# Performance work log

Hardware: AMD Instinct MI355X
Metric: run time of the kernel (lower is better)

## Reference

```python
import jax, jax.numpy as jnp
import numpy as np

T, N, L, H, COND, VOCAB = 64, 1024, 16, 256, 64, 100
HC = H + 1  # task_encoder hidden = hidden_size + 1
STATE = 1 + 1 + H + L + L  # a, v, h, a_probs, p


def gru_step(x, h, w_ih, w_hh, b_ih, b_hh):
    # PyTorch GRU/GRUCell gate math
    gi = x @ w_ih.T + b_ih
    gh = h @ w_hh.T + b_hh
    ir, iz, ig = jnp.split(gi, 3, axis=-1)
    hr, hz, hg = jnp.split(gh, 3, axis=-1)
    r = jax.nn.sigmoid(ir + hr)
    z = jax.nn.sigmoid(iz + hz)
    n = jnp.tanh(ig + r * hg)
    return (1.0 - z) * n + z * h


def setup_inputs():
    ks = jax.random.split(jax.random.key(0), 20)
    g = lambda i, sh: jax.random.normal(ks[i], sh, jnp.float32) * 0.05
    return {
        "condition": jax.random.normal(ks[0], (T, N, COND), jnp.float32),
        "lines": jax.random.randint(ks[1], (N, L), 0, VOCAB),
        "actions": jax.random.randint(ks[2], (T, N), 0, L),
        "rnn_hxs": jnp.zeros((N, STATE), jnp.float32),
        "emb": g(3, (VOCAB, H)),
        "w_ih_enc": g(4, (3 * HC, H)), "w_hh_enc": g(5, (3 * HC, HC)),
        "b_ih_enc": g(6, (3 * HC,)), "b_hh_enc": g(7, (3 * HC,)),
        "W1": g(8, (H, COND + H)), "b1": g(9, (H,)),
        "W2": g(10, (H, H)), "b2": g(11, (H,)),
        "w_ih_cell": g(12, (3 * H, H)), "w_hh_cell": g(13, (3 * H, H)),
        "b_ih_cell": g(14, (3 * H,)), "b_hh_cell": g(15, (3 * H,)),
        "Wa": g(16, (H, H)), "ba": g(17, (H,)),
        "Wc": g(18, (1, H)), "bc": g(19, (1,)),
    }


def _forward(condition, rnn_hxs, emb, w_ih_enc, w_hh_enc, b_ih_enc, b_hh_enc,
             W1, b1, W2, b2, w_ih_cell, w_hh_cell, b_ih_cell, b_hh_cell,
             Wa, ba, Wc, bc, lines, actions):
    n, l = lines.shape
    M = emb[lines]                     # [N, L, H]
    seq = jnp.transpose(M, (1, 0, 2))  # [L, N, H]
    idx = jnp.arange(l)

    # backward encoder: single scan over reversed sequence (outputs are causal,
    # so they equal torch's task_encoder(backward_input[:i]) for every i)
    def bstep(h, x):
        h2 = gru_step(x, h, w_ih_enc, w_hh_enc, b_ih_enc, b_hh_enc)
        return h2, h2
    _, B = jax.lax.scan(bstep, jnp.zeros((n, HC), M.dtype), seq[::-1])  # [L, N, HC]

    # forward encoder from every start i, batched over i with a start mask
    def fstep(carry, xj):
        x, j = xj
        h2 = gru_step(x, carry, w_ih_enc, w_hh_enc, b_ih_enc, b_hh_enc)  # [L(i), N, HC]
        h2 = jnp.where((j >= idx)[:, None, None], h2, carry)
        return h2, h2
    _, Fo = jax.lax.scan(fstep, jnp.zeros((l, n, HC), M.dtype), (seq, idx))  # [j, i, N, HC]
    Fo = jnp.transpose(Fo, (1, 0, 2, 3))                                     # [i, j, N, HC]

    # keys[i] = cat(flip(B[:i]), F_i)  ->  entry j<i is B[i-1-j], else forward enc
    bidx = jnp.clip(idx[:, None] - 1 - idx[None, :], 0, l - 1)  # [i, j]
    Kfull = jnp.where((idx[None, :] < idx[:, None])[:, :, None, None], B[bidx], Fo)
    Kfull = jnp.transpose(Kfull, (2, 0, 1, 3))  # [N, i, j, HC]
    K = Kfull[..., :H].sum(axis=1)              # [N, L, H]
    C = Kfull[..., H]                           # [N, i, j]

    _a, _v, h, _ap, p = jnp.split(rnn_hxs, [1, 2, 2 + H, 2 + H + l], axis=-1)
    new_ep = jnp.all(rnn_hxs == 0.0, axis=-1)
    p = p.at[:, 0].set(jnp.where(new_ep, 1.0, p[:, 0]))

    def step(carry, xs):
        h, p = carry
        cond_t, a_t = xs
        r = jnp.einsum('nl,nlh->nh', p, M)
        x = jnp.concatenate([cond_t, r], axis=-1)
        x = jax.nn.relu(x @ W1.T + b1)
        x = jax.nn.relu(x @ W2.T + b2)
        h = gru_step(x, h, w_ih_cell, w_hh_cell, b_ih_cell, b_hh_cell)
        k = h @ Wa.T + ba
        c = jnp.einsum('ni,nij->nj', p, C)
        w = jnp.einsum('nlh,nh->nl', K, k)
        probs = jax.nn.softmax(w * c, axis=-1)
        p_new = jax.nn.one_hot(a_t, l, dtype=h.dtype)  # actions >= 0 -> no resampling
        v = h @ Wc.T + bc
        out = jnp.concatenate([a_t[:, None].astype(h.dtype), v, h, probs, p_new], axis=-1)
        return (h, p_new), out

    _, hx = jax.lax.scan(step, (h, p), (condition, actions))  # [T, N, STATE]
    return hx


def reference(condition, lines, actions, rnn_hxs, emb, w_ih_enc, w_hh_enc, b_ih_enc, b_hh_enc, W1, b1, W2, b2, w_ih_cell, w_hh_cell, b_ih_cell, b_hh_cell, Wa, ba, Wc, bc):
    hx = _forward(condition, rnn_hxs, emb, w_ih_enc, w_hh_enc, b_ih_enc, b_hh_enc,
                  W1, b1, W2, b2, w_ih_cell, w_hh_cell, b_ih_cell, b_hh_cell,
                  Wa, ba, Wc, bc, lines, actions)
    return hx, hx[-1:]
```

## Files before the change

### kernel.cpp

```cpp
#include <hip/hip_runtime.h>
#include <hip/hip_bf16.h>
#include <cstddef>

#define T_ 64
#define N_ 1024
#define L_ 16
#define H_ 256
#define STATE_ 290
#define EKSTR 296

typedef short s16x8 __attribute__((ext_vector_type(8)));
typedef float f32x4 __attribute__((ext_vector_type(4)));
typedef ushort us4 __attribute__((ext_vector_type(4)));
typedef ushort us8 __attribute__((ext_vector_type(8)));
#define MFMA16 __builtin_amdgcn_mfma_f32_16x16x32_bf16

#define BAR() asm volatile("s_waitcnt lgkmcnt(0)\n\ts_barrier" ::: "memory")

__device__ __forceinline__ float b2f(ushort u){ return __uint_as_float(((unsigned)u) << 16); }
__device__ __forceinline__ ushort f2b(float f){
  unsigned x = __float_as_uint(f);
  return (ushort)((x + 0x7FFFu + ((x >> 16) & 1u)) >> 16);
}
__device__ __forceinline__ float gruh(float gir,float giz,float gig,
                                      float ghr,float ghz,float ghg,float hp){
  float r = 1.f/(1.f + __expf(-(gir + ghr)));
  float z = 1.f/(1.f + __expf(-(giz + ghz)));
  float g = tanhf(gig + r*ghg);
  return (1.f - z)*g + z*hp;
}

__global__ void prep_all(
    const float* __restrict__ wih_e, const float* __restrict__ whh_e,
    ushort* __restrict__ wihe_p, ushort* __restrict__ whhe_p,
    const float* __restrict__ wih_c, const float* __restrict__ whh_c,
    ushort* __restrict__ wihc_p, ushort* __restrict__ whhc_p,
    const float* __restrict__ bih_c, const float* __restrict__ bhh_c, float* __restrict__ cb,
    const float* __restrict__ W1, ushort* __restrict__ W1b,
    const float* __restrict__ W2, ushort* __restrict__ W2b,
    const float* __restrict__ Wa, ushort* __restrict__ WaTb){
  int b = blockIdx.x, t = threadIdx.x;
  if (b < 832) {
    int idx = b*256 + t;
    int d = idx >> 8, c = idx & 255;
    int tile = d >> 4, uu = d & 15;
    int k = tile/3, p = tile - 3*k;
    int hc = k*16 + uu;
    bool ok = (tile < 51) && (hc < 257);
    wihe_p[idx] = ok ? f2b(wih_e[(size_t)(p*257 + hc)*256 + c]) : (ushort)0;
  } else if (b < 1768) {
    int idx = (b-832)*256 + t;
    int d = idx / 288, c = idx - d*288;
    int tile = d >> 4, uu = d & 15;
    int k = tile/3, p = tile - 3*k;
    int hc = k*16 + uu;
    bool ok = (tile < 51) && (hc < 257) && (c < 257);
    whhe_p[idx] = ok ? f2b(whh_e[(size_t)(p*257 + hc)*257 + c]) : (ushort)0;
  } else if (b < 2536) {
    int idx = (b-1768)*256 + t;
    int d = idx >> 8, c = idx & 255;
    int tile = d >> 4, uu = d & 15;
    int k = tile/3, p = tile - 3*k;
    wihc_p[idx] = f2b(wih_c[(size_t)(p*256 + k*16 + uu)*256 + c]);
  } else if (b < 3304) {
    int idx = (b-2536)*256 + t;
    int d = idx >> 8, c = idx & 255;
    int tile = d >> 4, uu = d & 15;
    int k = tile/3, p = tile - 3*k;
    whhc_p[idx] = f2b(whh_c[(size_t)(p*256 + k*16 + uu)*256 + c]);
  } else if (b < 3307) {
    int d = (b-3304)*256 + t;
    if (d < 768) {
      int tile = d >> 4, uu = d & 15;
      int k = tile/3, p = tile - 3*k;
      int src = p*256 + k*16 + uu;
      cb[d] = bih_c[src] + (p < 2 ? bhh_c[src] : 0.f);
    }
  } else if (b < 3627) {
    int idx = (b-3307)*256 + t;
    W1b[idx] = f2b(W1[idx]);
  } else if (b < 3883) {
    int idx = (b-3627)*256 + t;
    W2b[idx] = f2b(W2[idx]);
  } else {
    int m = b - 3883;
    WaTb[(size_t)t*256 + m] = f2b(Wa[(size_t)m*256 + t]);
  }
}

__global__ void emb_init_r0(
    const int* __restrict__ lines, const float* __restrict__ emb, const float* __restrict__ hxs,
    ushort* __restrict__ Mbf, float* __restrict__ hbuf, float* __restrict__ p0,
    float* __restrict__ r0v){
  __shared__ ushort Ms[16][256];
  __shared__ float p0s[16];
  __shared__ int ls[16];
  __shared__ int nz;
  int n = blockIdx.x, t = threadIdx.x;
  if (t == 0) nz = 0;
  if (t < 16) ls[t] = lines[n*16 + t];
  __syncthreads();
  #pragma unroll
  for (int l = 0; l < 16; ++l) {
    ushort v = f2b(emb[(size_t)ls[l]*256 + t]);
    Ms[l][t] = v;
    Mbf[((size_t)n*16 + l)*256 + t] = v;
  }
  for (int c = t; c < STATE_; c += 256)
    if (hxs[(size_t)n*STATE_ + c] != 0.f) atomicOr(&nz, 1);
  __syncthreads();
  bool new_ep = (nz == 0);
  hbuf[(size_t)n*256 + t] = hxs[(size_t)n*STATE_ + 2 + t];
  if (t < 16) {
    float pv = hxs[(size_t)n*STATE_ + 2 + 256 + 16 + t];
    if (t == 0 && new_ep) pv = 1.f;
    p0[n*16 + t] = pv;
    p0s[t] = pv;
  }
  __syncthreads();
  float s = 0.f;
  #pragma unroll
  for (int l = 0; l < 16; ++l) s += p0s[l]*b2f(Ms[l][t]);
  r0v[(size_t)n*256 + t] = s;
}

__global__ void build_xcat8(const float* __restrict__ cond, const int* __restrict__ act,
                            const float* __restrict__ r0v, const ushort* __restrict__ Mbf,
                            ushort* __restrict__ xcat){
  int idx = blockIdx.x*256 + threadIdx.x;
  if (idx >= T_*N_*40) return;
  int kc = idx % 40;
  int row = idx / 40;
  int n = row & 1023, t = row >> 10;
  us8 v;
  if (kc < 8) {
    const float* cp = cond + (size_t)row*64 + kc*8;
    #pragma unroll
    for (int i = 0; i < 8; ++i) v[i] = f2b(cp[i]);
  } else if (t == 0) {
    const float* rp = r0v + (size_t)n*256 + (kc-8)*8;
    #pragma unroll
    for (int i = 0; i < 8; ++i) v[i] = f2b(rp[i]);
  } else {
    int a = act[(size_t)(t-1)*1024 + n];
    v = *(const us8*)(Mbf + ((size_t)n*16 + a)*256 + (kc-8)*8);
  }
  *(us8*)(xcat + (size_t)idx*8) = v;
}

template<int RELU>
__global__ __launch_bounds__(256) void gemm_mfma(
    const ushort* __restrict__ A, const ushort* __restrict__ W,
    const float* __restrict__ bias, ushort* __restrict__ out,
    int Kd, int ldo){
  __shared__ __align__(16) ushort Ws[64*328];
  int lane = threadIdx.x & 63, wv = threadIdx.x >> 6;
  int u = lane & 15, g4 = lane >> 4;
  int br = blockIdx.x*64 + wv*16;
  int bm = blockIdx.y*64;
  int ldw = Kd + 8;
  for (int i = threadIdx.x; i < 8*Kd; i += 256) {
    int e = i*8;
    int row = e / Kd, col = e - row*Kd;
    *(us8*)&Ws[row*ldw + col] = *(const us8*)(W + (size_t)(bm + row)*Kd + col);
  }
  __syncthreads();
  const ushort* Arow = A + (size_t)(br + u)*Kd + g4*8;
  f32x4 acc0 = {0,0,0,0}, acc1 = {0,0,0,0}, acc2 = {0,0,0,0}, acc3 = {0,0,0,0};
  for (int k0 = 0; k0 < Kd; k0 += 32) {
    s16x8 av = *(const s16x8*)(Arow + k0);
    s16x8 b0 = *(const s16x8*)&Ws[( 0 + u)*ldw + k0 + g4*8];
    s16x8 b1 = *(const s16x8*)&Ws[(16 + u)*ldw + k0 + g4*8];
    s16x8 b2 = *(const s16x8*)&Ws[(32 + u)*ldw + k0 + g4*8];
    s16x8 b3 = *(const s16x8*)&Ws[(48 + u)*ldw + k0 + g4*8];
    acc0 = MFMA16(av, b0, acc0, 0,0,0);
    acc1 = MFMA16(av, b1, acc1, 0,0,0);
    acc2 = MFMA16(av, b2, acc2, 0,0,0);
    acc3 = MFMA16(av, b3, acc3, 0,0,0);
  }
  f32x4 ac[4] = {acc0, acc1, acc2, acc3};
  #pragma unroll
  for (int mt = 0; mt < 4; ++mt) {
    int col = bm + mt*16 + u;
    float b = bias ? bias[col] : 0.f;
    #pragma unroll
    for (int r = 0; r < 4; ++r) {
      float v = ac[mt][r] + b;
      if (RELU) v = fmaxf(v, 0.f);
      out[(size_t)(br + g4*4 + r)*ldo + col] = f2b(v);
    }
  }
}

__global__ __launch_bounds__(512) __attribute__((amdgpu_waves_per_eu(2, 2))) void enc_all(
    const ushort* __restrict__ GiAll, const ushort* __restrict__ Wh,
    const float* __restrict__ bih, const float* __restrict__ bhh,
    float* __restrict__ Km, float* __restrict__ Cm, ushort* __restrict__ Bbf){
  __shared__ __align__(16) ushort hbf[2][80][EKSTR];
  __shared__ __align__(16) ushort gis[2][2][4][832];
  int tid = threadIdx.x, lane = tid & 63, wv = tid >> 6;
  int u = lane & 15, g4 = lane >> 4;
  int nb = blockIdx.x * 4;
  for (int i = tid; i < 2*80*EKSTR; i += 512) ((ushort*)hbf)[i] = 0;
  #pragma unroll
  for (int i0 = 0; i0 < 4; ++i0) {
    int i = tid + i0*512;
    if (i < 1664) {
      int flat = i*4;
      int fb = flat / 3328, rem = flat - fb*3328;
      int nl = rem / 832, k = rem - nl*832;
      int row = (nb+nl)*16 + (fb ? 15 : 0);
      *(us4*)&gis[0][fb][nl][k] = *(const us4*)(GiAll + (size_t)row*832 + k);
    }
  }
  BAR();
  int cur = 0;
  for (int j = 0; j < 16; ++j) {
    if (j < 15) {
      #pragma unroll
      for (int i0 = 0; i0 < 4; ++i0) {
        int i = tid + i0*512;
        if (i < 1664) {
          int flat = i*4;
          int fb = flat / 3328, rem = flat - fb*3328;
          int nl = rem / 832, k = rem - nl*832;
          int row = (nb+nl)*16 + (fb ? (14-j) : (j+1));
          *(us4*)&gis[cur^1][fb][nl][k] = *(const us4*)(GiAll + (size_t)row*832 + k);
        }
      }
    }
    #pragma unroll 1
    for (int tt = 0; tt < 2; ++tt) {
      int kt = 2*wv + tt;
      f32x4 acc[5][3];
      #pragma unroll
      for (int rt = 0; rt < 5; ++rt) {
        acc[rt][0] = (f32x4){0,0,0,0};
        acc[rt][1] = (f32x4){0,0,0,0};
        acc[rt][2] = (f32x4){0,0,0,0};
      }
      #pragma unroll
      for (int q = 0; q < 9; ++q) {
        int off = q*32 + g4*8;
        s16x8 w0 = *(const s16x8*)(Wh + (size_t)((3*kt+0)*16 + u)*288 + off);
        s16x8 w1 = *(const s16x8*)(Wh + (size_t)((3*kt+1)*16 + u)*288 + off);
        s16x8 w2 = *(const s16x8*)(Wh + (size_t)((3*kt+2)*16 + u)*288 + off);
        #pragma unroll
        for (int rt = 0; rt < 5; ++rt) {
          if (rt < 4 && rt*4 > j) continue;
          s16x8 av = *(const s16x8*)&hbf[cur][rt*16 + u][off];
          acc[rt][0] = MFMA16(av, w0, acc[rt][0], 0,0,0);
          acc[rt][1] = MFMA16(av, w1, acc[rt][1], 0,0,0);
          acc[rt][2] = MFMA16(av, w2, acc[rt][2], 0,0,0);
        }
      }
      int c = kt*16 + u;
      float bi0 = bih[c], bi1 = bih[257+c], bi2 = bih[514+c];
      float bh0 = bhh[c], bh1 = bhh[257+c], bh2 = bhh[514+c];
      float kmP[4] = {0.f, 0.f, 0.f, 0.f};
      #pragma unroll
      for (int rt = 0; rt < 4; ++rt) {
        int ii = rt*4 + g4;
        if (rt*4 <= j && ii <= j) {
          #pragma unroll
          for (int r = 0; r < 4; ++r) {
            int rowl = rt*16 + g4*4 + r;
            const ushort* gp = &gis[cur][0][r][3*kt*16];
            float hp = b2f(hbf[cur][rowl][c]);
            float h2 = gruh(b2f(gp[u]) + bi0, b2f(gp[16+u]) + bi1, b2f(gp[32+u]) + bi2,
                            acc[rt][0][r] + bh0, acc[rt][1][r] + bh1,
                            acc[rt][2][r] + bh2, hp);
            hbf[cur^1][rowl][c] = f2b(h2);
            kmP[r] += h2;
          }
        }
      }
      #pragma unroll
      for (int r = 0; r < 4; ++r) {
        float s = kmP[r];
        s += __shfl_xor(s, 16, 64);
        s += __shfl_xor(s, 32, 64);
        if (g4 == 0) Km[((size_t)(nb+r)*16 + j)*256 + c] = s;
      }
      if (g4 == 0) {
        #pragma unroll
        for (int r = 0; r < 4; ++r) {
          const ushort* gp = &gis[cur][1][r][3*kt*16];
          float hp = b2f(hbf[cur][64 + r][c]);
          float h2 = gruh(b2f(gp[u]) + bi0, b2f(gp[16+u]) + bi1, b2f(gp[32+u]) + bi2,
                          acc[4][0][r] + bh0, acc[4][1][r] + bh1,
                          acc[4][2][r] + bh2, hp);
          hbf[cur^1][64 + r][c] = f2b(h2);
          Bbf[((size_t)j*1024 + nb + r)*288 + c] = f2b(h2);
        }
      }
    }
    if (wv < 5) {
      int rt = wv;
      bool go = (rt == 4) || (rt*4 <= j);
      if (go) {
        f32x4 a0 = {0,0,0,0}, a1 = {0,0,0,0}, a2 = {0,0,0,0};
        #pragma unroll
        for (int q = 0; q < 9; ++q) {
          int off = q*32 + g4*8;
          s16x8 w0 = *(const s16x8*)(Wh + (size_t)(48*16 + u)*288 + off);
          s16x8 w1 = *(const s16x8*)(Wh + (size_t)(49*16 + u)*288 + off);
          s16x8 w2 = *(const s16x8*)(Wh + (size_t)(50*16 + u)*288 + off);
          s16x8 av = *(const s16x8*)&hbf[cur][rt*16 + u][off];
          a0 = MFMA16(av, w0, a0, 0,0,0);
          a1 = MFMA16(av, w1, a1, 0,0,0);
          a2 = MFMA16(av, w2, a2, 0,0,0);
        }
        if (u == 0) {
          float bi0 = bih[256], bi1 = bih[513], bi2 = bih[770];
          float bh0 = bhh[256], bh1 = bhh[513], bh2 = bhh[770];
          if (rt < 4) {
            int ii = rt*4 + g4;
            if (ii <= j) {
              #pragma unroll
              for (int r = 0; r < 4; ++r) {
                int rowl = rt*16 + g4*4 + r;
                const ushort* gp = &gis[cur][0][r][768];
                float hp = b2f(hbf[cur][rowl][256]);
                float h2 = gruh(b2f(gp[0]) + bi0, b2f(gp[16]) + bi1, b2f(gp[32]) + bi2,
                                a0[r] + bh0, a1[r] + bh1, a2[r] + bh2, hp);
                hbf[cur^1][rowl][256] = f2b(h2);
                Cm[(size_t)(nb+r)*256 + ii*16 + j] = h2;
              }
            }
          } else if (g4 == 0) {
            #pragma unroll
            for (int r = 0; r < 4; ++r) {
              const ushort* gp = &gis[cur][1][r][768];
              float hp = b2f(hbf[cur][64 + r][256]);
              float h2 = gruh(b2f(gp[0]) + bi0, b2f(gp[16]) + bi1, b2f(gp[32]) + bi2,
                              a0[r] + bh0, a1[r] + bh1, a2[r] + bh2, hp);
              hbf[cur^1][64 + r][256] = f2b(h2);
              Bbf[((size_t)j*1024 + nb + r)*288 + 256] = f2b(h2);
            }
          }
        }
      }
    }
    BAR();
    cur ^= 1;
  }
}

__global__ void accum_wb(const ushort* __restrict__ Bbf, const float* __restrict__ Km,
                         ushort* __restrict__ Kmbf, float* __restrict__ Cm,
                         const float* __restrict__ ba, float* __restrict__ wbv){
  __shared__ float kms[16][257];
  int n = blockIdx.x, c = threadIdx.x;
  float s = 0.f;
  for (int jj = 15; jj >= 0; --jj) {
    if (jj < 15) s += b2f(Bbf[((size_t)(14-jj)*1024 + n)*288 + c]);
    size_t o = ((size_t)n*16 + jj)*256 + c;
    float v = Km[o] + s;
    Kmbf[o] = f2b(v);
    kms[jj][c] = v;
  }
  int i = c >> 4, j = c & 15;
  if (i > j) Cm[(size_t)n*256 + i*16 + j] = b2f(Bbf[((size_t)(i-1-j)*1024 + n)*288 + 256]);
  __syncthreads();
  int l = c >> 4, lane16 = c & 15;
  float t = 0.f;
  for (int m = lane16; m < 256; m += 16) t += kms[l][m]*ba[m];
  t += __shfl_down(t, 8, 16); t += __shfl_down(t, 4, 16);
  t += __shfl_down(t, 2, 16); t += __shfl_down(t, 1, 16);
  if (lane16 == 0) wbv[n*16 + l] = t;
}

__global__ __launch_bounds__(512) __attribute__((amdgpu_waves_per_eu(2, 2))) void cell_chunk(
    const ushort* __restrict__ Gi, const ushort* __restrict__ Wh,
    const float* __restrict__ bhh, const float* __restrict__ hbuf,
    int t0, ushort* __restrict__ hcT, float* __restrict__ out){
  __shared__ __align__(16) ushort hbf[2][16][266];
  __shared__ __align__(16) ushort gis[2][16][768];
  int tid = threadIdx.x, lane = tid & 63, wv = tid >> 6;
  int u = lane & 15, g4 = lane >> 4;
  int n0 = blockIdx.x * 16;
  int ktA = wv, ktB = wv + 8;
  int cA = ktA*16 + u, cB = ktB*16 + u;
  s16x8 WA0[8], WA1[8], WA2[8], WB0[8], WB1[8], WB2[8];
  #pragma unroll
  for (int q = 0; q < 8; ++q) {
    int off = q*32 + g4*8;
    WA0[q] = *(const s16x8*)(Wh + (size_t)((3*ktA+0)*16 + u)*256 + off);
    WA1[q] = *(const s16x8*)(Wh + (size_t)((3*ktA+1)*16 + u)*256 + off);
    WA2[q] = *(const s16x8*)(Wh + (size_t)((3*ktA+2)*16 + u)*256 + off);
    WB0[q] = *(const s16x8*)(Wh + (size_t)((3*ktB+0)*16 + u)*256 + off);
    WB1[q] = *(const s16x8*)(Wh + (size_t)((3*ktB+1)*16 + u)*256 + off);
    WB2[q] = *(const s16x8*)(Wh + (size_t)((3*ktB+2)*16 + u)*256 + off);
  }
  float bhgA = bhh[512 + cA], bhgB = bhh[512 + cB];
  if (t0 == 0) {
    for (int i = tid; i < 16*256; i += 512) {
      int rr = i >> 8, cc = i & 255;
      hbf[0][rr][cc] = f2b(hbuf[(size_t)(n0 + rr)*256 + cc]);
    }
  } else {
    for (int i = tid; i < 16*256; i += 512) {
      int rr = i >> 8, cc = i & 255;
      hbf[0][rr][cc] = hcT[((size_t)(t0-1)*1024 + n0 + rr)*256 + cc];
    }
  }
  for (int i = tid; i < 1536; i += 512)
    *(us8*)&((ushort*)gis[0])[i*8] = *(const us8*)(Gi + (size_t)n0*768 + i*8);
  BAR();
  int cur = 0;
  for (int s = 0; s < 16; ++s) {
    int t = t0 + s;
    if (s < 15) {
      const ushort* src = Gi + (size_t)(s+1)*1024*768 + (size_t)n0*768;
      for (int i = tid; i < 1536; i += 512)
        *(us8*)&((ushort*)gis[cur^1])[i*8] = *(const us8*)(src + i*8);
    }
    f32x4 a0={0,0,0,0},a1={0,0,0,0},a2={0,0,0,0};
    f32x4 b0={0,0,0,0},b1={0,0,0,0},b2={0,0,0,0};
    #pragma unroll
    for (int q = 0; q < 8; ++q) {
      s16x8 ah = *(const s16x8*)&hbf[cur][u][q*32 + g4*8];
      a0 = MFMA16(ah, WA0[q], a0, 0,0,0);
      a1 = MFMA16(ah, WA1[q], a1, 0,0,0);
      a2 = MFMA16(ah, WA2[q], a2, 0,0,0);
      b0 = MFMA16(ah, WB0[q], b0, 0,0,0);
      b1 = MFMA16(ah, WB1[q], b1, 0,0,0);
      b2 = MFMA16(ah, WB2[q], b2, 0,0,0);
    }
    #pragma unroll
    for (int r = 0; r < 4; ++r) {
      int row = g4*4 + r;
      const ushort* gr = &gis[cur][row][0];
      {
        float gir = b2f(gr[3*ktA*16 + u]);
        float giz = b2f(gr[3*ktA*16 + 16 + u]);
        float gig = b2f(gr[3*ktA*16 + 32 + u]);
        float hp  = b2f(hbf[cur][row][cA]);
        float rr2 = 1.f/(1.f + __expf(-(gir + a0[r])));
        float zz  = 1.f/(1.f + __expf(-(giz + a1[r])));
        float ex  = __expf(2.f*(gig + rr2*(a2[r] + bhgA)));
        float gg  = 1.f - 2.f/(ex + 1.f);
        float h2  = (1.f - zz)*gg + zz*hp;
        ushort hb = f2b(h2);
        hbf[cur^1][row][cA] = hb;
        hcT[((size_t)t*1024 + n0 + row)*256 + cA] = hb;
        out[((size_t)t*1024 + n0 + row)*STATE_ + 2 + cA] = h2;
        if (t == 63) out[((size_t)64*1024 + n0 + row)*STATE_ + 2 + cA] = h2;
      }
      {
        float gir = b2f(gr[3*ktB*16 + u]);
        float giz = b2f(gr[3*ktB*16 + 16 + u]);
        float gig = b2f(gr[3*ktB*16 + 32 + u]);
        float hp  = b2f(hbf[cur][row][cB]);
        float rr2 = 1.f/(1.f + __expf(-(gir + b0[r])));
        float zz  = 1.f/(1.f + __expf(-(giz + b1[r])));
        float ex  = __expf(2.f*(gig + rr2*(b2[r] + bhgB)));
        float gg  = 1.f - 2.f/(ex + 1.f);
        float h2  = (1.f - zz)*gg + zz*hp;
        ushort hb = f2b(h2);
        hbf[cur^1][row][cB] = hb;
        hcT[((size_t)t*1024 + n0 + row)*256 + cB] = hb;
        out[((size_t)t*1024 + n0 + row)*STATE_ + 2 + cB] = h2;
        if (t == 63) out[((size_t)64*1024 + n0 + row)*STATE_ + 2 + cB] = h2;
      }
    }
    BAR();
    cur ^= 1;
  }
}

__global__ __launch_bounds__(256) void attn_v(
    const ushort* __restrict__ Ktl, const ushort* __restrict__ hcT,
    const float* __restrict__ wbv, const float* __restrict__ Cm,
    const float* __restrict__ p0, const int* __restrict__ act,
    const float* __restrict__ Wc, const float* __restrict__ bc,
    float* __restrict__ out){
  __shared__ float WcS[256];
  int n = blockIdx.x;
  int tid = threadIdx.x;
  WcS[tid] = Wc[tid];
  __syncthreads();
  int lane = tid & 63, wv = tid >> 6;
  int u = lane & 15, g4 = lane >> 4;
  int t0 = wv*16;
  const ushort* Ka = Ktl + ((size_t)n*16 + u)*256 + g4*8;
  const ushort* Hb = hcT + ((size_t)(t0 + u)*1024 + n)*256 + g4*8;
  f32x4 acc = {0,0,0,0};
  float vp = 0.f;
  #pragma unroll
  for (int q = 0; q < 8; ++q) {
    s16x8 av = *(const s16x8*)(Ka + q*32);
    s16x8 bv = *(const s16x8*)(Hb + q*32);
    acc = MFMA16(av, bv, acc, 0,0,0);
    #pragma unroll
    for (int j = 0; j < 8; ++j) vp += b2f((ushort)bv[j]) * WcS[q*32 + g4*8 + j];
  }
  vp += __shfl_xor(vp, 16, 64);
  vp += __shfl_xor(vp, 32, 64);
  float vfin = vp + bc[0];
  int t = t0 + u;
  float ps[4];
  if (t == 0) {
    #pragma unroll
    for (int r = 0; r < 4; ++r) {
      float catt = 0.f;
      for (int i = 0; i < 16; ++i) catt += p0[n*16 + i]*Cm[(size_t)n*256 + i*16 + g4*4 + r];
      ps[r] = (acc[r] + wbv[n*16 + g4*4 + r]) * catt;
    }
  } else {
    int ap = act[(size_t)(t-1)*1024 + n];
    #pragma unroll
    for (int r = 0; r < 4; ++r)
      ps[r] = (acc[r] + wbv[n*16 + g4*4 + r]) * Cm[(size_t)n*256 + ap*16 + g4*4 + r];
  }
  float mx = fmaxf(fmaxf(ps[0], ps[1]), fmaxf(ps[2], ps[3]));
  mx = fmaxf(mx, __shfl_xor(mx, 16, 64));
  mx = fmaxf(mx, __shfl_xor(mx, 32, 64));
  float e[4], se = 0.f;
  #pragma unroll
  for (int r = 0; r < 4; ++r) { e[r] = __expf(ps[r] - mx); se += e[r]; }
  se += __shfl_xor(se, 16, 64);
  se += __shfl_xor(se, 32, 64);
  float inv = 1.f/se;
  int a = act[(size_t)t*1024 + n];
  size_t ro = ((size_t)t*1024 + n)*STATE_;
  if (g4 == 0) { out[ro] = (float)a; out[ro + 1] = vfin; }
  #pragma unroll
  for (int r = 0; r < 4; ++r) {
    out[ro + 258 + g4*4 + r] = e[r]*inv;
    out[ro + 274 + g4*4 + r] = (g4*4 + r == a) ? 1.f : 0.f;
  }
  if (t == 63) {
    size_t r2 = ((size_t)64*1024 + n)*STATE_;
    if (g4 == 0) { out[r2] = (float)a; out[r2 + 1] = vfin; }
    #pragma unroll
    for (int r = 0; r < 4; ++r) {
      out[r2 + 258 + g4*4 + r] = e[r]*inv;
      out[r2 + 274 + g4*4 + r] = (g4*4 + r == a) ? 1.f : 0.f;
    }
  }
}

extern "C" void kernel_launch(void* const* d_in, const int* in_sizes, int n_in,
                              void* d_out, int out_size, void* d_ws, size_t ws_size,
                              hipStream_t stream){
  (void)in_sizes; (void)n_in; (void)out_size; (void)ws_size;
  const float* cond  = (const float*)d_in[0];
  const int*   lines = (const int*)  d_in[1];
  const int*   act   = (const int*)  d_in[2];
  const float* hxs   = (const float*)d_in[3];
  const float* emb   = (const float*)d_in[4];
  const float* wih_e = (const float*)d_in[5];
  const float* whh_e = (const float*)d_in[6];
  const float* bih_e = (const float*)d_in[7];
  const float* bhh_e = (const float*)d_in[8];
  const float* W1    = (const float*)d_in[9];
  const float* b1    = (const float*)d_in[10];
  const float* W2    = (const float*)d_in[11];
  const float* b2    = (const float*)d_in[12];
  const float* wih_c = (const float*)d_in[13];
  const float* whh_c = (const float*)d_in[14];
  const float* bih_c = (const float*)d_in[15];
  const float* bhh_c = (const float*)d_in[16];
  const float* Wa    = (const float*)d_in[17];
  const float* ba    = (const float*)d_in[18];
  const float* Wc    = (const float*)d_in[19];
  const float* bc    = (const float*)d_in[20];
  float* out = (float*)d_out;

  char* base = (char*)d_ws;
  ushort* Mbf    = (ushort*)(base + 0);
  ushort* Bbf    = (ushort*)(base + 8388608);
  float*  Km     = (float*) (base + 17825792);
  ushort* Kmbf   = (ushort*)(base + 34603008);
  ushort* xcat   = (ushort*)(base + 8388608);
  ushort* x2     = (ushort*)(base + 8388608);
  ushort* hcT    = (ushort*)(base + 8388608);
  ushort* GiAll  = (ushort*)(base + 50331648);
  ushort* x1     = (ushort*)(base + 50331648);
  ushort* GiC0   = (ushort*)(base + 50331648);
  ushort* GiC1   = (ushort*)(base + 75497472);
  ushort* Ktl    = (ushort*)(base + 100663296);
  float*  Cm     = (float*) (base + 109051904);
  float*  hbuf   = (float*) (base + 110100480);
  float*  p0     = (float*) (base + 111149056);
  float*  r0v    = (float*) (base + 111214592);
  float*  wbv    = (float*) (base + 112263168);
  ushort* wihe_p = (ushort*)(base + 112328704);
  ushort* whhe_p = (ushort*)(base + 112754688);
  ushort* wihc_p = (ushort*)(base + 113233920);
  ushort* whhc_p = (ushort*)(base + 113627136);
  ushort* W1b    = (ushort*)(base + 114020352);
  ushort* W2b    = (ushort*)(base + 114184192);
  ushort* WaTb   = (ushort*)(base + 114315264);
  float*  cbias  = (float*) (base + 114446336);

  prep_all<<<4139, 256, 0, stream>>>(wih_e, whh_e, wihe_p, whhe_p,
                                     wih_c, whh_c, wihc_p, whhc_p,
                                     bih_c, bhh_c, cbias, W1, W1b, W2, W2b, Wa, WaTb);
  emb_init_r0<<<1024, 256, 0, stream>>>(lines, emb, hxs, Mbf, hbuf, p0, r0v);

  gemm_mfma<0><<<dim3(256, 13), 256, 0, stream>>>(Mbf, wihe_p, nullptr, GiAll, 256, 832);
  enc_all<<<256, 512, 0, stream>>>(GiAll, whhe_p, bih_e, bhh_e, Km, Cm, Bbf);
  accum_wb<<<1024, 256, 0, stream>>>(Bbf, Km, Kmbf, Cm, ba, wbv);
  gemm_mfma<0><<<dim3(256, 4), 256, 0, stream>>>(Kmbf, WaTb, nullptr, Ktl, 256, 256);

  build_xcat8<<<10240, 256, 0, stream>>>(cond, act, r0v, Mbf, xcat);
  gemm_mfma<1><<<dim3(1024, 4), 256, 0, stream>>>(xcat, W1b, b1, x1, 320, 256);
  gemm_mfma<1><<<dim3(1024, 4), 256, 0, stream>>>(x1, W2b, b2, x2, 256, 256);

  ushort* gic[2] = {GiC0, GiC1};
  gemm_mfma<0><<<dim3(256, 12), 256, 0, stream>>>(x2 + (size_t)0*16384*256, wihc_p, cbias, gic[0], 256, 768);
  gemm_mfma<0><<<dim3(256, 12), 256, 0, stream>>>(x2 + (size_t)1*16384*256, wihc_p, cbias, gic[1], 256, 768);
  cell_chunk<<<64, 512, 0, stream>>>(gic[0], whhc_p, bhh_c, hbuf,  0, hcT, out);
  gemm_mfma<0><<<dim3(256, 12), 256, 0, stream>>>(x2 + (size_t)2*16384*256, wihc_p, cbias, gic[0], 256, 768);
  cell_chunk<<<64, 512, 0, stream>>>(gic[1], whhc_p, bhh_c, hbuf, 16, hcT, out);
  gemm_mfma<0><<<dim3(256, 12), 256, 0, stream>>>(x2 + (size_t)3*16384*256, wihc_p, cbias, gic[1], 256, 768);
  cell_chunk<<<64, 512, 0, stream>>>(gic[0], whhc_p, bhh_c, hbuf, 32, hcT, out);
  cell_chunk<<<64, 512, 0, stream>>>(gic[1], whhc_p, bhh_c, hbuf, 48, hcT, out);

  attn_v<<<1024, 256, 0, stream>>>(Ktl, hcT, wbv, Cm, p0, act, Wc, bc, out);
}
```

Baseline: 884.4 us.

## Keep encoder recurrent weights in registers and precompute Gi load addressing

In the encoder kernel, each wave now loads its first tile's recurrent weight fragments once into registers before the 16-step loop and reloads only the second tile's weights each step, instead of reloading both from global every step. The per-step Gi staging address arithmetic (divisions by 832/3328) is hoisted into precomputed pointers, and tanhf is replaced by an exp-based formula. This removes repeated global weight traffic and integer/transcendental overhead, at the cost of much higher VGPR pressure under the fixed two-waves-per-EU limit, which risks spills.

```diff
diff --git a/kernel.cpp b/kernel.cpp
--- a/kernel.cpp
+++ b/kernel.cpp
@@ -21,13 +21,6 @@
 __device__ __forceinline__ ushort f2b(float f){
   unsigned x = __float_as_uint(f);
   return (ushort)((x + 0x7FFFu + ((x >> 16) & 1u)) >> 16);
-}
-__device__ __forceinline__ float gruh(float gir,float giz,float gig,
-                                      float ghr,float ghz,float ghg,float hp){
-  float r = 1.f/(1.f + __expf(-(gir + ghr)));
-  float z = 1.f/(1.f + __expf(-(giz + ghz)));
-  float g = tanhf(gig + r*ghg);
-  return (1.f - z)*g + z*hp;
 }
 
 __global__ void prep_all(
@@ -192,6 +185,74 @@
   }
 }
 
+__device__ __forceinline__ void enc_pass(
+    int j, int nb, int u, int g4, int cur, int c, int g3off,
+    float bi0, float bi1, float bi2, float bh0, float bh1, float bh2,
+    const s16x8 (&w0)[9], const s16x8 (&w1)[9], const s16x8 (&w2)[9],
+    ushort hbf[2][80][EKSTR], const ushort gis[2][2][4][832],
+    float* __restrict__ Km, ushort* __restrict__ Bbf){
+  f32x4 acc[5][3];
+  #pragma unroll
+  for (int rt = 0; rt < 5; ++rt) {
+    acc[rt][0] = (f32x4){0,0,0,0};
+    acc[rt][1] = (f32x4){0,0,0,0};
+    acc[rt][2] = (f32x4){0,0,0,0};
+  }
+  #pragma unroll
+  for (int q = 0; q < 9; ++q) {
+    int off = q*32 + g4*8;
+    #pragma unroll
+    for (int rt = 0; rt < 5; ++rt) {
+      if (rt < 4 && rt*4 > j) continue;
+      s16x8 av = *(const s16x8*)&hbf[cur][rt*16 + u][off];
+      acc[rt][0] = MFMA16(av, w0[q], acc[rt][0], 0,0,0);
+      acc[rt][1] = MFMA16(av, w1[q], acc[rt][1], 0,0,0);
+      acc[rt][2] = MFMA16(av, w2[q], acc[rt][2], 0,0,0);
+    }
+  }
+  float kmP[4] = {0.f, 0.f, 0.f, 0.f};
+  #pragma unroll
+  for (int rt = 0; rt < 4; ++rt) {
+    int ii = rt*4 + g4;
+    if (rt*4 <= j && ii <= j) {
+      #pragma unroll
+      for (int r = 0; r < 4; ++r) {
+        int rowl = rt*16 + g4*4 + r;
+        const ushort* gp = &gis[cur][0][r][g3off];
+        float hp = b2f(hbf[cur][rowl][c]);
+        float rr = 1.f/(1.f + __expf(-(b2f(gp[u]) + bi0 + acc[rt][0][r] + bh0)));
+        float zz = 1.f/(1.f + __expf(-(b2f(gp[16+u]) + bi1 + acc[rt][1][r] + bh1)));
+        float ex = __expf(2.f*(b2f(gp[32+u]) + bi2 + rr*(acc[rt][2][r] + bh2)));
+        float gg = 1.f - 2.f/(ex + 1.f);
+        float h2 = (1.f - zz)*gg + zz*hp;
+        hbf[cur^1][rowl][c] = f2b(h2);
+        kmP[r] += h2;
+      }
+    }
+  }
+  #pragma unroll
+  for (int r = 0; r < 4; ++r) {
+    float s = kmP[r];
+    s += __shfl_xor(s, 16, 64);
+    s += __shfl_xor(s, 32, 64);
+    if (g4 == 0) Km[((size_t)(nb+r)*16 + j)*256 + c] = s;
+  }
+  if (g4 == 0) {
+    #pragma unroll
+    for (int r = 0; r < 4; ++r) {
+      const ushort* gp = &gis[cur][1][r][g3off];
+      float hp = b2f(hbf[cur][64 + r][c]);
+      float rr = 1.f/(1.f + __expf(-(b2f(gp[u]) + bi0 + acc[4][0][r] + bh0)));
+      float zz = 1.f/(1.f + __expf(-(b2f(gp[16+u]) + bi1 + acc[4][1][r] + bh1)));
+      float ex = __expf(2.f*(b2f(gp[32+u]) + bi2 + rr*(acc[4][2][r] + bh2)));
+      float gg = 1.f - 2.f/(ex + 1.f);
+      float h2 = (1.f - zz)*gg + zz*hp;
+      hbf[cur^1][64 + r][c] = f2b(h2);
+      Bbf[((size_t)j*1024 + nb + r)*288 + c] = f2b(h2);
+    }
+  }
+}
+
 __global__ __launch_bounds__(512) __attribute__((amdgpu_waves_per_eu(2, 2))) void enc_all(
     const ushort* __restrict__ GiAll, const ushort* __restrict__ Wh,
     const float* __restrict__ bih, const float* __restrict__ bhh,
@@ -202,98 +263,63 @@
   int u = lane & 15, g4 = lane >> 4;
   int nb = blockIdx.x * 4;
   for (int i = tid; i < 2*80*EKSTR; i += 512) ((ushort*)hbf)[i] = 0;
-  #pragma unroll
-  for (int i0 = 0; i0 < 4; ++i0) {
-    int i = tid + i0*512;
-    if (i < 1664) {
-      int flat = i*4;
-      int fb = flat / 3328, rem = flat - fb*3328;
-      int nl = rem / 832, k = rem - nl*832;
-      int row = (nb+nl)*16 + (fb ? 15 : 0);
-      *(us4*)&gis[0][fb][nl][k] = *(const us4*)(GiAll + (size_t)row*832 + k);
-    }
-  }
+  int i0c = tid;                 bool fb0 = (i0c*4) >= 3328;
+  int i1c = tid + 512;           bool fb1 = (i1c*4) >= 3328;
+  int i2c = tid + 1024;          bool fb2 = (i2c*4) >= 3328;
+  int i3c = tid + 1536;          bool fb3 = (i3c*4) >= 3328; bool gv3 = (i3c < 1664);
+  int r0c = i0c*4 - (fb0 ? 3328 : 0), nl0 = r0c/832, k0c = r0c - nl0*832;
+  int r1c = i1c*4 - (fb1 ? 3328 : 0), nl1 = r1c/832, k1c = r1c - nl1*832;
+  int r2c = i2c*4 - (fb2 ? 3328 : 0), nl2 = r2c/832, k2c = r2c - nl2*832;
+  int r3c = i3c*4 - (fb3 ? 3328 : 0), nl3 = r3c/832, k3c = r3c - nl3*832;
+  const ushort* gs0 = GiAll + ((size_t)(nb+nl0)*16)*832 + k0c;
+  const ushort* gs1 = GiAll + ((size_t)(nb+nl1)*16)*832 + k1c;
+  const ushort* gs2 = GiAll + ((size_t)(nb+nl2)*16)*832 + k2c;
+  const ushort* gs3 = GiAll + ((size_t)(nb+nl3)*16)*832 + k3c;
+  ushort* gd0 = ((ushort*)gis) + (fb0 ? 3328 : 0) + nl0*832 + k0c;
+  ushort* gd1 = ((ushort*)gis) + (fb1 ? 3328 : 0) + nl1*832 + k1c;
+  ushort* gd2 = ((ushort*)gis) + (fb2 ? 3328 : 0) + nl2*832 + k2c;
+  ushort* gd3 = ((ushort*)gis) + (fb3 ? 3328 : 0) + nl3*832 + k3c;
+  *(us4*)gd0 = *(const us4*)(gs0 + (fb0 ? 15 : 0)*832);
+  *(us4*)gd1 = *(const us4*)(gs1 + (fb1 ? 15 : 0)*832);
+  *(us4*)gd2 = *(const us4*)(gs2 + (fb2 ? 15 : 0)*832);
+  if (gv3) *(us4*)gd3 = *(const us4*)(gs3 + (fb3 ? 15 : 0)*832);
+  int ktA = 2*wv, ktB = 2*wv + 1;
+  s16x8 wA0[9], wA1[9], wA2[9];
+  #pragma unroll
+  for (int q = 0; q < 9; ++q) {
+    int off = q*32 + g4*8;
+    wA0[q] = *(const s16x8*)(Wh + (size_t)((3*ktA+0)*16 + u)*288 + off);
+    wA1[q] = *(const s16x8*)(Wh + (size_t)((3*ktA+1)*16 + u)*288 + off);
+    wA2[q] = *(const s16x8*)(Wh + (size_t)((3*ktA+2)*16 + u)*288 + off);
+  }
+  int cAe = ktA*16 + u, cBe = cAe + 16;
+  float biA0 = bih[cAe], biA1 = bih[257+cAe], biA2 = bih[514+cAe];
+  float bhA0 = bhh[cAe], bhA1 = bhh[257+cAe], bhA2 = bhh[514+cAe];
+  float biB0 = bih[cBe], biB1 = bih[257+cBe], biB2 = bih[514+cBe];
+  float bhB0 = bhh[cBe], bhB1 = bhh[257+cBe], bhB2 = bhh[514+cBe];
   BAR();
   int cur = 0;
   for (int j = 0; j < 16; ++j) {
     if (j < 15) {
-      #pragma unroll
-      for (int i0 = 0; i0 < 4; ++i0) {
-        int i = tid + i0*512;
-        if (i < 1664) {
-          int flat = i*4;
-          int fb = flat / 3328, rem = flat - fb*3328;
-          int nl = rem / 832, k = rem - nl*832;
-          int row = (nb+nl)*16 + (fb ? (14-j) : (j+1));
-          *(us4*)&gis[cur^1][fb][nl][k] = *(const us4*)(GiAll + (size_t)row*832 + k);
-        }
-      }
-    }
-    #pragma unroll 1
-    for (int tt = 0; tt < 2; ++tt) {
-      int kt = 2*wv + tt;
-      f32x4 acc[5][3];
-      #pragma unroll
-      for (int rt = 0; rt < 5; ++rt) {
-        acc[rt][0] = (f32x4){0,0,0,0};
-        acc[rt][1] = (f32x4){0,0,0,0};
-        acc[rt][2] = (f32x4){0,0,0,0};
-      }
+      int bufo = (cur^1)*6656;
+      *(us4*)(gd0 + bufo) = *(const us4*)(gs0 + (fb0 ? (14-j) : (j+1))*832);
+      *(us4*)(gd1 + bufo) = *(const us4*)(gs1 + (fb1 ? (14-j) : (j+1))*832);
+      *(us4*)(gd2 + bufo) = *(const us4*)(gs2 + (fb2 ? (14-j) : (j+1))*832);
+      if (gv3) *(us4*)(gd3 + bufo) = *(const us4*)(gs3 + (fb3 ? (14-j) : (j+1))*832);
+    }
+    enc_pass(j, nb, u, g4, cur, cAe, 3*ktA*16,
+             biA0, biA1, biA2, bhA0, bhA1, bhA2, wA0, wA1, wA2, hbf, gis, Km, Bbf);
+    {
+      s16x8 wB0[9], wB1[9], wB2[9];
       #pragma unroll
       for (int q = 0; q < 9; ++q) {
         int off = q*32 + g4*8;
-        s16x8 w0 = *(const s16x8*)(Wh + (size_t)((3*kt+0)*16 + u)*288 + off);
-        s16x8 w1 = *(const s16x8*)(Wh + (size_t)((3*kt+1)*16 + u)*288 + off);
-        s16x8 w2 = *(const s16x8*)(Wh + (size_t)((3*kt+2)*16 + u)*288 + off);
-        #pragma unroll
-        for (int rt = 0; rt < 5; ++rt) {
-          if (rt < 4 && rt*4 > j) continue;
-          s16x8 av = *(const s16x8*)&hbf[cur][rt*16 + u][off];
-          acc[rt][0] = MFMA16(av, w0, acc[rt][0], 0,0,0);
-          acc[rt][1] = MFMA16(av, w1, acc[rt][1], 0,0,0);
-          acc[rt][2] = MFMA16(av, w2, acc[rt][2], 0,0,0);
-        }
+        wB0[q] = *(const s16x8*)(Wh + (size_t)((3*ktB+0)*16 + u)*288 + off);
+        wB1[q] = *(const s16x8*)(Wh + (size_t)((3*ktB+1)*16 + u)*288 + off);
+        wB2[q] = *(const s16x8*)(Wh + (size_t)((3*ktB+2)*16 + u)*288 + off);
       }
-      int c = kt*16 + u;
-      float bi0 = bih[c], bi1 = bih[257+c], bi2 = bih[514+c];
-      float bh0 = bhh[c], bh1 = bhh[257+c], bh2 = bhh[514+c];
-      float kmP[4] = {0.f, 0.f, 0.f, 0.f};
-      #pragma unroll
-      for (int rt = 0; rt < 4; ++rt) {
-        int ii = rt*4 + g4;
-        if (rt*4 <= j && ii <= j) {
-          #pragma unroll
-          for (int r = 0; r < 4; ++r) {
-            int rowl = rt*16 + g4*4 + r;
-            const ushort* gp = &gis[cur][0][r][3*kt*16];
-            float hp = b2f(hbf[cur][rowl][c]);
-            float h2 = gruh(b2f(gp[u]) + bi0, b2f(gp[16+u]) + bi1, b2f(gp[32+u]) + bi2,
-                            acc[rt][0][r] + bh0, acc[rt][1][r] + bh1,
-                            acc[rt][2][r] + bh2, hp);
-            hbf[cur^1][rowl][c] = f2b(h2);
-            kmP[r] += h2;
-          }
-        }
-      }
-      #pragma unroll
-      for (int r = 0; r < 4; ++r) {
-        float s = kmP[r];
-        s += __shfl_xor(s, 16, 64);
-        s += __shfl_xor(s, 32, 64);
-        if (g4 == 0) Km[((size_t)(nb+r)*16 + j)*256 + c] = s;
-      }
-      if (g4 == 0) {
-        #pragma unroll
-        for (int r = 0; r < 4; ++r) {
-          const ushort* gp = &gis[cur][1][r][3*kt*16];
-          float hp = b2f(hbf[cur][64 + r][c]);
-          float h2 = gruh(b2f(gp[u]) + bi0, b2f(gp[16+u]) + bi1, b2f(gp[32+u]) + bi2,
-                          acc[4][0][r] + bh0, acc[4][1][r] + bh1,
-                          acc[4][2][r] + bh2, hp);
-          hbf[cur^1][64 + r][c] = f2b(h2);
-          Bbf[((size_t)j*1024 + nb + r)*288 + c] = f2b(h2);
-        }
-      }
+      enc_pass(j, nb, u, g4, cur, cBe, 3*ktB*16,
+               biB0, biB1, biB2, bhB0, bhB1, bhB2, wB0, wB1, wB2, hbf, gis, Km, Bbf);
     }
     if (wv < 5) {
       int rt = wv;
@@ -322,8 +348,11 @@
                 int rowl = rt*16 + g4*4 + r;
                 const ushort* gp = &gis[cur][0][r][768];
                 float hp = b2f(hbf[cur][rowl][256]);
-                float h2 = gruh(b2f(gp[0]) + bi0, b2f(gp[16]) + bi1, b2f(gp[32]) + bi2,
-                                a0[r] + bh0, a1[r] + bh1, a2[r] + bh2, hp);
+                float rr = 1.f/(1.f + __expf(-(b2f(gp[0]) + bi0 + a0[r] + bh0)));
+                float zz = 1.f/(1.f + __expf(-(b2f(gp[16]) + bi1 + a1[r] + bh1)));
+                float ex = __expf(2.f*(b2f(gp[32]) + bi2 + rr*(a2[r] + bh2)));
+                float gg = 1.f - 2.f/(ex + 1.f);
+                float h2 = (1.f - zz)*gg + zz*hp;
                 hbf[cur^1][rowl][256] = f2b(h2);
                 Cm[(size_t)(nb+r)*256 + ii*16 + j] = h2;
               }
@@ -333,8 +362,11 @@
             for (int r = 0; r < 4; ++r) {
               const ushort* gp = &gis[cur][1][r][768];
               float hp = b2f(hbf[cur][64 + r][256]);
-              float h2 = gruh(b2f(gp[0]) + bi0, b2f(gp[16]) + bi1, b2f(gp[32]) + bi2,
-                              a0[r] + bh0, a1[r] + bh1, a2[r] + bh2, hp);
+              float rr = 1.f/(1.f + __expf(-(b2f(gp[0]) + bi0 + a0[r] + bh0)));
+              float zz = 1.f/(1.f + __expf(-(b2f(gp[16]) + bi1 + a1[r] + bh1)));
+              float ex = __expf(2.f*(b2f(gp[32]) + bi2 + rr*(a2[r] + bh2)));
+              float gg = 1.f - 2.f/(ex + 1.f);
+              float h2 = (1.f - zz)*gg + zz*hp;
               hbf[cur^1][64 + r][256] = f2b(h2);
               Bbf[((size_t)j*1024 + nb + r)*288 + 256] = f2b(h2);
             }
```

After: 1.047 ms. +18.3%, slower.
